# Kernel tuning notes

Measured on AMD Instinct MI355X. Metric: run time of the kernel, lower is better.

Reference implementation:

```python
import jax, jax.numpy as jnp
import numpy as np

DN = ('NCHW', 'OIHW', 'NCHW')
WINDOW_SIZES = (11, 25, 49)


def conv(x, w, b=None, pad=0, groups=1):
    y = jax.lax.conv_general_dilated(
        x, w, window_strides=(1, 1), padding=((pad, pad), (pad, pad)),
        dimension_numbers=DN, feature_group_count=groups)
    if b is not None:
        y = y + b[None, :, None, None]
    return y


def box_mean(f, wsize):
    # depthwise box-filter local mean with reflect padding (matches F.pad mode='reflect')
    C = f.shape[1]
    p = wsize // 2
    fp = jnp.pad(f, ((0, 0), (0, 0), (p, p), (p, p)), mode='reflect')
    k = jnp.ones((C, 1, wsize, wsize), f.dtype) / (wsize * wsize)
    return conv(fp, k, groups=C)


def std_map(features, wsize):
    # per-channel local std, channel-weighted sum, then **0.8
    C = features.shape[1]
    # C == 8 here, so weights are softmax(ones) == uniform (torch path for C != 4)
    cw = jax.nn.softmax(jnp.ones((C,), features.dtype))
    m = box_mean(features, wsize)
    m2 = box_mean(features ** 2, wsize)
    var = jnp.clip(m2 - m ** 2, 1e-6, None)
    res = jnp.sum(cw[None, :, None, None] * jnp.sqrt(var), axis=1, keepdims=True)
    return res ** 0.8  # [B,1,H,W]


def setup_inputs() -> dict:
    key = jax.random.key(0)
    ks = jax.random.split(key, 8)
    B, C, H, W = 8, 4, 512, 512
    x = jax.random.normal(ks[0], (B, C, H, W), dtype=jnp.float32)
    conv1_w = jax.random.normal(ks[1], (32, 4, 3, 3), dtype=jnp.float32) * 0.1
    conv1_b = jnp.zeros((32,), jnp.float32)
    conv2_w = jax.random.normal(ks[2], (16, 32, 3, 3), dtype=jnp.float32) * 0.05
    conv2_b = jnp.zeros((16,), jnp.float32)
    conv3_w = jax.random.normal(ks[3], (8, 16, 3, 3), dtype=jnp.float32) * 0.05
    conv3_b = jnp.zeros((8,), jnp.float32)
    # scale_fusion init: weight = 1/len(window_sizes), bias = 0
    fusion_w = jnp.full((1, len(WINDOW_SIZES), 1, 1), 1.0 / len(WINDOW_SIZES), jnp.float32)
    fusion_b = jnp.zeros((1,), jnp.float32)
    channel_weights = jnp.ones((4,), jnp.float32) / 4.0
    return dict(x=x, conv1_w=conv1_w, conv1_b=conv1_b, conv2_w=conv2_w,
                conv2_b=conv2_b, conv3_w=conv3_w, conv3_b=conv3_b,
                fusion_w=fusion_w, fusion_b=fusion_b,
                channel_weights=channel_weights)


def reference(x, conv1_w, conv1_b, conv2_w, conv2_b, conv3_w, conv3_b,
              fusion_w, fusion_b, channel_weights):
    lrelu = lambda v: jnp.where(v >= 0, v, 0.2 * v)
    # feature extractor: conv3x3 -> lrelu -> conv3x3 -> lrelu -> conv3x3
    f = lrelu(conv(x, conv1_w, conv1_b, pad=1))
    f = lrelu(conv(f, conv2_w, conv2_b, pad=1))
    f = conv(f, conv3_w, conv3_b, pad=1)  # [B,8,H,W]
    # multi-scale std maps
    maps = [std_map(f, w) for w in WINDOW_SIZES]
    multi = jnp.concatenate(maps, axis=1)  # [B,3,H,W]
    fused = jax.nn.relu(conv(multi, fusion_w, fusion_b, pad=0))  # [B,1,H,W]
    # adaptive thresholds (global quantiles over the whole fused std map)
    qs = jnp.quantile(fused.reshape(-1), jnp.array([0.25, 0.75], fused.dtype))
    q25, q75 = qs[0], qs[1]
    iqr = q75 - q25
    gstd = jnp.std(x, axis=(2, 3), keepdims=True, ddof=1)  # [B,4,1,1] (torch unbiased)
    lo = (q25 - 0.5 * iqr) * jnp.ones_like(gstd)
    hi = (q75 + 0.5 * iqr) * jnp.ones_like(gstd)
    gf = jnp.clip(gstd * 5.0, 0.5, 2.0)
    lo, hi = lo * gf, hi * gf
    cw = jax.nn.softmax(channel_weights)[None, :, None, None]
    cstd = jnp.std(x * cw, axis=(2, 3), keepdims=True, ddof=1)
    cf = jnp.clip(cstd * 2.0, 0.8, 1.2)
    lo, hi = lo * cf, hi * cf
    # mask generation: broadcast [B,1,H,W] vs [B,4,1,1] -> [B,4,H,W], then mean over C
    n = jnp.clip((fused - lo) / (hi - lo), 0.0, 1.0)
    mask = jax.nn.sigmoid(6.0 * n - 3.0)
    return jnp.mean(mask, axis=1, keepdims=True)  # [B,1,H,W]
```

## Files before the change

kernel.cpp:

```cpp
#include <hip/hip_runtime.h>
#include <cmath>

#define HH 512
#define WW 512
#define NB 8
#define CIN 4
#define C2 32
#define C3 16
#define CF 8
#define HW (HH*WW)
#define NPIX (NB*HW)
#define NBC 2

__device__ __forceinline__ float lrelu_f(float v){ return v < 0.f ? 0.2f*v : v; }
__device__ __forceinline__ int reflect_i(int i){ int r = i < 0 ? -i : i; return r >= HH ? 2*HH - 2 - r : r; }

template<int Ci, int Co, bool LRELU>
__global__ __launch_bounds__(256) void k_conv8(const float* __restrict__ in,
                                               const float* __restrict__ wgt,
                                               const float* __restrict__ bias,
                                               float* __restrict__ outp)
{
    constexpr int NG = Co/8;
    __shared__ float wl[Co*Ci*9];
    __shared__ float bl[Co];
    for (int i = threadIdx.x; i < Co*Ci*9; i += 256) wl[i] = wgt[i];
    if (threadIdx.x < Co) bl[threadIdx.x] = bias[threadIdx.x];
    __syncthreads();

    int bid   = blockIdx.x;
    int local = bid % (NG*128);
    int b     = bid / (NG*128);
    int cb    = local & 3;
    int rb    = (local >> 2) & 31;
    int cg    = local >> 7;
    int tid   = threadIdx.x;
    int lane  = tid & 31;
    int col   = cb*128 + lane*4;
    int row0  = rb*16  + (tid >> 5)*2;
    int co0   = cg*8;
    const float* inb = in + (size_t)b*Ci*HW;

    float acc[8][2][4];
    #pragma unroll
    for (int j=0;j<8;j++){
        float bv = bl[co0+j];
        #pragma unroll
        for (int r=0;r<2;r++)
            #pragma unroll
            for (int p=0;p<4;p++) acc[j][r][p] = bv;
    }

    #pragma unroll 2
    for (int ci=0; ci<Ci; ci++){
        float v[4][6];
        const float* inc = inb + (size_t)ci*HW;
        #pragma unroll
        for (int dy=0;dy<4;dy++){
            int hh = row0 + dy - 1;
            int hc = hh < 0 ? 0 : (hh > HH-1 ? HH-1 : hh);
            bool hok = (unsigned)hh < (unsigned)HH;
            const float* rowp = inc + hc*WW;
            float4 m = *(const float4*)(rowp + col);
            float lft = 0.f, rgt = 0.f;
            if (lane == 0  && col > 0)      lft = rowp[col-1];
            if (lane == 31 && col+4 < WW)   rgt = rowp[col+4];
            float v0 = __shfl_up(m.w, 1, 32);
            float v5 = __shfl_down(m.x, 1, 32);
            if (lane == 0)  v0 = lft;
            if (lane == 31) v5 = rgt;
            if (!hok){ m.x=0.f; m.y=0.f; m.z=0.f; m.w=0.f; v0=0.f; v5=0.f; }
            v[dy][0]=v0; v[dy][1]=m.x; v[dy][2]=m.y;
            v[dy][3]=m.z; v[dy][4]=m.w; v[dy][5]=v5;
        }
        #pragma unroll
        for (int j=0;j<8;j++){
            const float* wr = &wl[((co0+j)*Ci + ci)*9];
            float wj[9];
            #pragma unroll
            for (int q=0;q<9;q++) wj[q] = wr[q];
            #pragma unroll
            for (int dy=0;dy<3;dy++){
                #pragma unroll
                for (int dx=0;dx<3;dx++){
                    float wv = wj[dy*3+dx];
                    #pragma unroll
                    for (int r=0;r<2;r++)
                        #pragma unroll
                        for (int p=0;p<4;p++)
                            acc[j][r][p] = fmaf(v[dy+r][dx+p], wv, acc[j][r][p]);
                }
            }
        }
    }

    float* ob = outp + (size_t)b*Co*HW;
    #pragma unroll
    for (int j=0;j<8;j++){
        #pragma unroll
        for (int r=0;r<2;r++){
            float4 o;
            o.x = LRELU ? lrelu_f(acc[j][r][0]) : acc[j][r][0];
            o.y = LRELU ? lrelu_f(acc[j][r][1]) : acc[j][r][1];
            o.z = LRELU ? lrelu_f(acc[j][r][2]) : acc[j][r][2];
            o.w = LRELU ? lrelu_f(acc[j][r][3]) : acc[j][r][3];
            *(float4*)(ob + (size_t)(co0+j)*HW + (size_t)(row0+r)*WW + col) = o;
        }
    }
}

template<int WS, bool FIRST>
__global__ __launch_bounds__(256) void k_vhbox(const float* __restrict__ f,
                                               float* __restrict__ fused,
                                               const float* __restrict__ fwv, int sidx)
{
    constexpr int P    = WS/2;
    constexpr int SW   = ((256 + 2*P + 31)/32)*32;
    constexpr int SEGC = SW/32;
    constexpr int SVW  = (SW + (SW>>4) + 3) | 1;
    constexpr int RSW  = 256 + 16 + 2;
    constexpr float inv = 1.f/((float)WS*(float)WS);

    __shared__ float sv[CF*SVW];
    __shared__ float sq[CF*SVW];
    __shared__ float resv[CF*RSW];

    int bid  = blockIdx.x;
    int band = bid & 31;
    int half = (bid >> 5) & 1;
    int b    = bid >> 6;
    int r0   = band*16;
    int c0   = half*256;
    int tid  = threadIdx.x;
    int ch   = tid >> 5;
    int seg  = tid & 31;

    const float* fp = f + (size_t)(b*CF + ch)*HW;

    int rc[SEGC];
    #pragma unroll
    for (int k = 0; k < SEGC; k++){
        int gc = c0 - P + k*32 + seg;
        gc = gc < 0 ? -gc : (gc > WW-1 ? 2*WW-2 - gc : gc);
        rc[k] = gc;
    }

    float vsr[SEGC], vqr[SEGC];
    #pragma unroll
    for (int k = 0; k < SEGC; k++){ vsr[k]=0.f; vqr[k]=0.f; }
    for (int dy = -P; dy <= P; dy++){
        const float* rp = fp + (size_t)reflect_i(r0+dy)*WW;
        #pragma unroll
        for (int k = 0; k < SEGC; k++){
            float v = rp[rc[k]];
            vsr[k] += v; vqr[k] = fmaf(v, v, vqr[k]);
        }
    }

    float fwb = fwv[sidx];

    for (int rr = 0; rr < 16; rr++){
        __syncthreads();
        #pragma unroll
        for (int k = 0; k < SEGC; k++){
            int j = k*32 + seg; int sj = j + (j>>4);
            sv[ch*SVW + sj] = vsr[k];
            sq[ch*SVW + sj] = vqr[k];
        }
        float ev[SEGC], lv[SEGC];
        if (rr < 15){
            const float* ep = fp + (size_t)reflect_i(r0+rr+1+P)*WW;
            const float* lp = fp + (size_t)reflect_i(r0+rr-P)*WW;
            #pragma unroll
            for (int k = 0; k < SEGC; k++){ ev[k]=ep[rc[k]]; lv[k]=lp[rc[k]]; }
        }
        __syncthreads();
        int oc0 = seg*8;
        float S = 0.f, Q = 0.f;
        #pragma unroll
        for (int k = 0; k < WS; k++){
            int j = oc0 + k; int sj = j + (j>>4);
            S += sv[ch*SVW + sj];
            Q += sq[ch*SVW + sj];
        }
        float res[8];
        #pragma unroll
        for (int t = 0; t < 8; t++){
            float m  = S*inv, m2 = Q*inv;
            float var = fmaxf(fmaf(-m, m, m2), 1e-6f);
            res[t] = sqrtf(var);
            if (t < 7){
                int ja = oc0 + t + WS, jb = oc0 + t;
                S += sv[ch*SVW + ja + (ja>>4)] - sv[ch*SVW + jb + (jb>>4)];
                Q += sq[ch*SVW + ja + (ja>>4)] - sq[ch*SVW + jb + (jb>>4)];
            }
        }
        #pragma unroll
        for (int t = 0; t < 8; t++){
            int j = oc0 + t;
            resv[ch*RSW + j + (j>>4)] = res[t];
        }
        if (rr < 15){
            #pragma unroll
            for (int k = 0; k < SEGC; k++){
                vsr[k] += ev[k] - lv[k];
                vqr[k] = fmaf(ev[k], ev[k], vqr[k]);
                vqr[k] = fmaf(-lv[k], lv[k], vqr[k]);
            }
        }
        __syncthreads();
        int colI = tid;
        float a = 0.f;
        #pragma unroll
        for (int cc = 0; cc < CF; cc++) a += resv[cc*RSW + colI + (colI>>4)];
        float val = fwb * powf(a*0.125f, 0.8f);
        size_t oi = ((size_t)b*HH + r0 + rr)*WW + c0 + colI;
        if (FIRST) fused[oi] = val; else fused[oi] += val;
    }
}

__global__ void k_h8(const float* __restrict__ fused, const float* __restrict__ fb,
                     unsigned* __restrict__ hist8)
{
    __shared__ unsigned lh[256];
    lh[threadIdx.x] = 0;
    __syncthreads();
    float fbv = fb[0];
    int i = blockIdx.x*256 + threadIdx.x;
    int stride = gridDim.x*256;
    for (; i < NPIX; i += stride){
        float v = fmaxf(fused[i] + fbv, 0.f);
        atomicAdd(&lh[__float_as_uint(v) >> 24], 1u);
    }
    __syncthreads();
    if (lh[threadIdx.x]) atomicAdd(&hist8[threadIdx.x], lh[threadIdx.x]);
}

__global__ void k_scan8(const unsigned* __restrict__ hist8,
                        int* __restrict__ cand8, int* __restrict__ rank8)
{
    if (threadIdx.x == 0){
        const unsigned RK[4] = {524287u, 524288u, 1572863u, 1572864u};
        unsigned cum = 0; int qi = 0;
        for (int b = 0; b < 256 && qi < 4; b++){
            unsigned cnt = hist8[b];
            while (qi < 4 && RK[qi] < cum + cnt){
                cand8[qi] = b; rank8[qi] = (int)(RK[qi] - cum); qi++;
            }
            cum += cnt;
        }
    }
}

__global__ void k_h8b(const float* __restrict__ fused, const float* __restrict__ fb,
                      const int* __restrict__ cand8, unsigned* __restrict__ hist8b)
{
    __shared__ unsigned lh[1024];
    for (int i = threadIdx.x; i < 1024; i += 256) lh[i] = 0;
    __syncthreads();
    float fbv = fb[0];
    int c0 = cand8[0], c1 = cand8[1], c2 = cand8[2], c3 = cand8[3];
    bool d1 = (c1 != c0);
    bool d2 = (c2 != c0) && (c2 != c1);
    bool d3 = (c3 != c0) && (c3 != c1) && (c3 != c2);
    int i = blockIdx.x*256 + threadIdx.x;
    int stride = gridDim.x*256;
    for (; i < NPIX; i += stride){
        unsigned u = __float_as_uint(fmaxf(fused[i] + fbv, 0.f));
        int hi = (int)(u >> 24);
        unsigned mid = (u >> 16) & 0xffu;
        if (hi == c0)       atomicAdd(&lh[mid],       1u);
        if (d1 && hi == c1) atomicAdd(&lh[256u+mid],  1u);
        if (d2 && hi == c2) atomicAdd(&lh[512u+mid],  1u);
        if (d3 && hi == c3) atomicAdd(&lh[768u+mid],  1u);
    }
    __syncthreads();
    for (int i = threadIdx.x; i < 1024; i += 256)
        if (lh[i]) atomicAdd(&hist8b[i], lh[i]);
}

__global__ void k_scan8b(const unsigned* __restrict__ hist8b,
                         const int* __restrict__ cand8, const int* __restrict__ rank8,
                         int* __restrict__ cand16, int* __restrict__ rank16)
{
    int qi = threadIdx.x;
    if (qi < 4){
        int slot = qi;
        for (int j = 0; j < qi; j++) if (cand8[j] == cand8[qi]){ slot = j; break; }
        const unsigned* h = hist8b + slot*256;
        unsigned k = (unsigned)rank8[qi], cum = 0;
        for (int b = 0; b < 256; b++){
            unsigned cnt = h[b];
            if (cnt && k >= cum && k < cum + cnt){
                cand16[qi] = (cand8[qi] << 8) | b;
                rank16[qi] = (int)(k - cum);
            }
            cum += cnt;
        }
    }
}

__global__ void k_h16(const float* __restrict__ fused, const float* __restrict__ fb,
                      const int* __restrict__ cand16, unsigned* __restrict__ histlo)
{
    float fbv = fb[0];
    int c0 = cand16[0], c1 = cand16[1], c2 = cand16[2], c3 = cand16[3];
    bool d1 = (c1 != c0);
    bool d2 = (c2 != c0) && (c2 != c1);
    bool d3 = (c3 != c0) && (c3 != c1) && (c3 != c2);
    int i = blockIdx.x*256 + threadIdx.x;
    int stride = gridDim.x*256;
    for (; i < NPIX; i += stride){
        unsigned u = __float_as_uint(fmaxf(fused[i] + fbv, 0.f));
        int hi = (int)(u >> 16);
        unsigned lo = u & 0xffffu;
        if (hi == c0)       atomicAdd(&histlo[lo],           1u);
        if (d1 && hi == c1) atomicAdd(&histlo[65536u + lo],  1u);
        if (d2 && hi == c2) atomicAdd(&histlo[131072u + lo], 1u);
        if (d3 && hi == c3) atomicAdd(&histlo[196608u + lo], 1u);
    }
}

__global__ void k_scan16(const unsigned* __restrict__ histlo,
                         const int* __restrict__ cand16, const int* __restrict__ rank16,
                         float* __restrict__ ostat)
{
    int qi = blockIdx.x;
    int slot = qi;
    for (int j = 0; j < qi; j++) if (cand16[j] == cand16[qi]){ slot = j; break; }
    const unsigned* hist = histlo + (size_t)slot*65536;
    __shared__ unsigned csum[256];
    __shared__ unsigned cbase[256];
    int t = threadIdx.x;
    unsigned s = 0;
    for (int i = 0; i < 256; i++) s += hist[t*256 + i];
    csum[t] = s;
    __syncthreads();
    if (t == 0){ unsigned run = 0; for (int i = 0; i < 256; i++){ cbase[i] = run; run += csum[i]; } }
    __syncthreads();
    unsigned k = (unsigned)rank16[qi];
    unsigned cum = cbase[t];
    for (int i = 0; i < 256; i++){
        unsigned cnt = hist[t*256 + i];
        if (cnt && k >= cum && k < cum + cnt)
            ostat[qi] = __uint_as_float(((unsigned)cand16[qi] << 16) | (unsigned)(t*256 + i));
        cum += cnt;
    }
}

__global__ void k_gstd_part(const float* __restrict__ x, double* __restrict__ part)
{
    int bid = blockIdx.x;
    int plane = bid >> 3, chunk = bid & 7;
    const float4* p4 = (const float4*)(x + (size_t)plane*HW + (size_t)chunk*32768);
    int t = threadIdx.x;
    double s=0.0, s2=0.0;
    for (int k=0;k<32;k++){
        float4 v = p4[k*256 + t];
        s  += (double)v.x + (double)v.y + (double)v.z + (double)v.w;
        s2 += (double)v.x*v.x + (double)v.y*v.y + (double)v.z*v.z + (double)v.w*v.w;
    }
    __shared__ double rs[256], rq[256];
    rs[t]=s; rq[t]=s2; __syncthreads();
    for (int off=128; off>0; off>>=1){
        if (t<off){ rs[t]+=rs[t+off]; rq[t]+=rq[t+off]; }
        __syncthreads();
    }
    if (t==0){ part[bid*2]=rs[0]; part[bid*2+1]=rq[0]; }
}

__global__ void k_gstd_final(const double* __restrict__ part, float* __restrict__ gstd)
{
    int t = threadIdx.x;
    if (t < 32){
        double s=0.0, s2=0.0;
        for (int j=0;j<8;j++){ s += part[(t*8+j)*2]; s2 += part[(t*8+j)*2+1]; }
        const double N = 262144.0;
        double var = (s2 - s*s/N) / (N - 1.0);
        gstd[t] = (float)sqrt(var < 0.0 ? 0.0 : var);
    }
}

__global__ void k_finalize(const float* __restrict__ ostat, const float* __restrict__ gstd,
                           const float* __restrict__ cwin, float* __restrict__ lov, float* __restrict__ hiv)
{
    int t = threadIdx.x;
    if (t < 32){
        float q25 = ostat[0] + 0.75f*(ostat[1]-ostat[0]);
        float q75 = ostat[2] + 0.25f*(ostat[3]-ostat[2]);
        float iqr = q75 - q25;
        float lo_b = q25 - 0.5f*iqr, hi_b = q75 + 0.5f*iqr;
        int c = t & 3;
        float m = fmaxf(fmaxf(cwin[0],cwin[1]), fmaxf(cwin[2],cwin[3]));
        float e0 = expf(cwin[0]-m), e1 = expf(cwin[1]-m), e2 = expf(cwin[2]-m), e3 = expf(cwin[3]-m);
        float smc = expf(cwin[c]-m) / (e0+e1+e2+e3);
        float g  = gstd[t];
        float gf = fminf(fmaxf(g*5.f, 0.5f), 2.f);
        float cf = fminf(fmaxf(smc*g*2.f, 0.8f), 1.2f);
        lov[t] = lo_b*gf*cf;
        hiv[t] = hi_b*gf*cf;
    }
}

__global__ void k_mask(const float* __restrict__ fused_in, const float* __restrict__ fb,
                       const float* __restrict__ lov, const float* __restrict__ hiv,
                       float* __restrict__ outp)
{
    int i = blockIdx.x*256 + threadIdx.x;
    float F = fmaxf(fused_in[i] + fb[0], 0.f);
    int b = i >> 18;
    float o = 0.f;
    #pragma unroll
    for (int c=0;c<4;c++){
        float lo = lov[b*4+c], hi = hiv[b*4+c];
        float n = (F - lo) / (hi - lo);
        n = fminf(fmaxf(n, 0.f), 1.f);
        o += 1.f/(1.f + expf(3.f - 6.f*n));
    }
    outp[i] = 0.25f * o;
}

extern "C" void kernel_launch(void* const* d_in, const int* in_sizes, int n_in,
                              void* d_out, int out_size, void* d_ws, size_t ws_size,
                              hipStream_t stream)
{
    const float* x  = (const float*)d_in[0];
    const float* w1 = (const float*)d_in[1];
    const float* b1 = (const float*)d_in[2];
    const float* w2 = (const float*)d_in[3];
    const float* b2 = (const float*)d_in[4];
    const float* w3 = (const float*)d_in[5];
    const float* b3 = (const float*)d_in[6];
    const float* fw = (const float*)d_in[7];
    const float* fb = (const float*)d_in[8];
    const float* cw = (const float*)d_in[9];
    float* out = (float*)d_out;
    char* ws = (char*)d_ws;

    size_t off = 0;
    auto take = [&](size_t bytes)->size_t{ size_t o = off; off += (bytes + 255) & ~(size_t)255; return o; };
    size_t o_h8     = take(256*4);
    size_t o_h8b    = take(1024*4);
    size_t o_histlo = take((size_t)4*65536*4);
    size_t o_c8     = take(4*4);
    size_t o_r8     = take(4*4);
    size_t o_c16    = take(4*4);
    size_t o_r16    = take(4*4);
    size_t o_os     = take(4*4);
    size_t o_part   = take(512*8);
    size_t o_gs     = take(32*4);
    size_t o_lo     = take(32*4);
    size_t o_hi     = take(32*4);
    size_t o_R1     = take((size_t)NB*C3*HW*4);
    size_t o_R2     = take((size_t)NBC*C2*HW*4);

    float*    f2buf  = (float*)(ws + o_R1);
    float*    f1     = (float*)(ws + o_R2);
    float*    fbuf   = (float*)(ws + o_R2);
    unsigned* hist8  = (unsigned*)(ws + o_h8);
    unsigned* hist8b = (unsigned*)(ws + o_h8b);
    unsigned* histlo = (unsigned*)(ws + o_histlo);
    int*      c8     = (int*)(ws + o_c8);
    int*      r8     = (int*)(ws + o_r8);
    int*      c16    = (int*)(ws + o_c16);
    int*      r16    = (int*)(ws + o_r16);
    float*    osv    = (float*)(ws + o_os);
    double*   part   = (double*)(ws + o_part);
    float*    gs     = (float*)(ws + o_gs);
    float*    lov    = (float*)(ws + o_lo);
    float*    hiv    = (float*)(ws + o_hi);

    for (int ck = 0; ck < NB/NBC; ck++){
        const float* xb = x + (size_t)ck*NBC*CIN*HW;
        k_conv8<CIN,C2,true ><<<NBC*512,256,0,stream>>>(xb, w1, b1, f1);
        k_conv8<C2, C3,true ><<<NBC*256,256,0,stream>>>(f1, w2, b2,
                                                        f2buf + (size_t)ck*NBC*C3*HW);
    }
    k_conv8<C3, CF, false><<<NB*128,256,0,stream>>>(f2buf, w3, b3, fbuf);

    k_gstd_part<<<256,256,0,stream>>>(x, part);
    k_gstd_final<<<1,256,0,stream>>>(part, gs);

    const int bgrid = NB*2*32;
    k_vhbox<11,true ><<<bgrid,256,0,stream>>>(fbuf, out, fw, 0);
    k_vhbox<25,false><<<bgrid,256,0,stream>>>(fbuf, out, fw, 1);
    k_vhbox<49,false><<<bgrid,256,0,stream>>>(fbuf, out, fw, 2);

    hipMemsetAsync(hist8,  0, 256*4,  stream);
    hipMemsetAsync(hist8b, 0, 1024*4, stream);
    hipMemsetAsync(histlo, 0, (size_t)4*65536*4, stream);
    k_h8    <<<2048,256,0,stream>>>(out, fb, hist8);
    k_scan8 <<<1,64,0,stream>>>(hist8, c8, r8);
    k_h8b   <<<2048,256,0,stream>>>(out, fb, c8, hist8b);
    k_scan8b<<<1,64,0,stream>>>(hist8b, c8, r8, c16, r16);
    k_h16   <<<2048,256,0,stream>>>(out, fb, c16, histlo);
    k_scan16<<<4,256,0,stream>>>(histlo, c16, r16, osv);

    k_finalize<<<1,64,0,stream>>>(osv, gs, cw, lov, hiv);
    k_mask<<<NPIX/256,256,0,stream>>>(out, fb, lov, hiv, out);
}
```

Before: 905.9 us.

## Fuse three std-map scales into one kernel and shrink conv tiles

The three per-scale box-filter std kernels are merged into one kernel that reads a shared 320-wide padded strip and keeps running column sums for all three windows. This removes two passes over the feature map and the read-modify-write of the fused output. The conv kernels now compute one row per thread instead of two, doubling the grid, and conv3 runs inside the batch-chunk loop so intermediates stay smaller. The three histogram memsets are also collapsed into one. The cost is higher register pressure in the fused std kernel, plus lost row reuse in the conv kernels.

```diff
diff --git a/kernel.cpp b/kernel.cpp
--- a/kernel.cpp
+++ b/kernel.cpp
@@ -12,11 +12,17 @@
 #define NPIX (NB*HW)
 #define NBC 2
 
+#define SEGC 10
+#define SW   320
+#define SVW  ((SW + (SW>>4) + 3) | 1)
+#define RSW  (256 + 16 + 2)
+
 __device__ __forceinline__ float lrelu_f(float v){ return v < 0.f ? 0.2f*v : v; }
 __device__ __forceinline__ int reflect_i(int i){ int r = i < 0 ? -i : i; return r >= HH ? 2*HH - 2 - r : r; }
+__device__ __forceinline__ int swz(int j){ return j + (j >> 4); }
 
 template<int Ci, int Co, bool LRELU>
-__global__ __launch_bounds__(256) void k_conv8(const float* __restrict__ in,
+__global__ __launch_bounds__(256) void k_conv4(const float* __restrict__ in,
                                                const float* __restrict__ wgt,
                                                const float* __restrict__ bias,
                                                float* __restrict__ outp)
@@ -29,42 +35,40 @@
     __syncthreads();
 
     int bid   = blockIdx.x;
-    int local = bid % (NG*128);
-    int b     = bid / (NG*128);
+    int local = bid % (NG*256);
+    int b     = bid / (NG*256);
     int cb    = local & 3;
-    int rb    = (local >> 2) & 31;
-    int cg    = local >> 7;
+    int rb    = (local >> 2) & 63;
+    int cg    = local >> 8;
     int tid   = threadIdx.x;
     int lane  = tid & 31;
     int col   = cb*128 + lane*4;
-    int row0  = rb*16  + (tid >> 5)*2;
+    int row   = rb*8 + (tid >> 5);
     int co0   = cg*8;
     const float* inb = in + (size_t)b*Ci*HW;
 
-    float acc[8][2][4];
+    float acc[8][4];
     #pragma unroll
     for (int j=0;j<8;j++){
         float bv = bl[co0+j];
         #pragma unroll
-        for (int r=0;r<2;r++)
-            #pragma unroll
-            for (int p=0;p<4;p++) acc[j][r][p] = bv;
+        for (int p=0;p<4;p++) acc[j][p] = bv;
     }
 
     #pragma unroll 2
     for (int ci=0; ci<Ci; ci++){
-        float v[4][6];
+        float v[3][6];
         const float* inc = inb + (size_t)ci*HW;
         #pragma unroll
-        for (int dy=0;dy<4;dy++){
-            int hh = row0 + dy - 1;
+        for (int dy=0;dy<3;dy++){
+            int hh = row + dy - 1;
             int hc = hh < 0 ? 0 : (hh > HH-1 ? HH-1 : hh);
             bool hok = (unsigned)hh < (unsigned)HH;
             const float* rowp = inc + hc*WW;
             float4 m = *(const float4*)(rowp + col);
             float lft = 0.f, rgt = 0.f;
-            if (lane == 0  && col > 0)      lft = rowp[col-1];
-            if (lane == 31 && col+4 < WW)   rgt = rowp[col+4];
+            if (lane == 0  && col > 0)    lft = rowp[col-1];
+            if (lane == 31 && col+4 < WW) rgt = rowp[col+4];
             float v0 = __shfl_up(m.w, 1, 32);
             float v5 = __shfl_down(m.x, 1, 32);
             if (lane == 0)  v0 = lft;
@@ -85,10 +89,8 @@
                 for (int dx=0;dx<3;dx++){
                     float wv = wj[dy*3+dx];
                     #pragma unroll
-                    for (int r=0;r<2;r++)
-                        #pragma unroll
-                        for (int p=0;p<4;p++)
-                            acc[j][r][p] = fmaf(v[dy+r][dx+p], wv, acc[j][r][p]);
+                    for (int p=0;p<4;p++)
+                        acc[j][p] = fmaf(v[dy][dx+p], wv, acc[j][p]);
                 }
             }
         }
@@ -97,33 +99,71 @@
     float* ob = outp + (size_t)b*Co*HW;
     #pragma unroll
     for (int j=0;j<8;j++){
-        #pragma unroll
-        for (int r=0;r<2;r++){
-            float4 o;
-            o.x = LRELU ? lrelu_f(acc[j][r][0]) : acc[j][r][0];
-            o.y = LRELU ? lrelu_f(acc[j][r][1]) : acc[j][r][1];
-            o.z = LRELU ? lrelu_f(acc[j][r][2]) : acc[j][r][2];
-            o.w = LRELU ? lrelu_f(acc[j][r][3]) : acc[j][r][3];
-            *(float4*)(ob + (size_t)(co0+j)*HW + (size_t)(row0+r)*WW + col) = o;
-        }
-    }
-}
-
-template<int WS, bool FIRST>
-__global__ __launch_bounds__(256) void k_vhbox(const float* __restrict__ f,
-                                               float* __restrict__ fused,
-                                               const float* __restrict__ fwv, int sidx)
-{
-    constexpr int P    = WS/2;
-    constexpr int SW   = ((256 + 2*P + 31)/32)*32;
-    constexpr int SEGC = SW/32;
-    constexpr int SVW  = (SW + (SW>>4) + 3) | 1;
-    constexpr int RSW  = 256 + 16 + 2;
+        float4 o;
+        o.x = LRELU ? lrelu_f(acc[j][0]) : acc[j][0];
+        o.y = LRELU ? lrelu_f(acc[j][1]) : acc[j][1];
+        o.z = LRELU ? lrelu_f(acc[j][2]) : acc[j][2];
+        o.w = LRELU ? lrelu_f(acc[j][3]) : acc[j][3];
+        *(float4*)(ob + (size_t)(co0+j)*HW + (size_t)row*WW + col) = o;
+    }
+}
+
+template<int WS>
+__device__ __forceinline__ float scale_step(float2* __restrict__ svq,
+                                            float* __restrict__ resv,
+                                            const float* vs, const float* vq,
+                                            float fws)
+{
+    constexpr int P   = WS/2;
+    constexpr int OFF = 24 - P;
     constexpr float inv = 1.f/((float)WS*(float)WS);
-
-    __shared__ float sv[CF*SVW];
-    __shared__ float sq[CF*SVW];
-    __shared__ float resv[CF*RSW];
+    const int tid = threadIdx.x;
+    const int ch  = tid >> 5;
+    const int seg = tid & 31;
+
+    __syncthreads();
+    #pragma unroll
+    for (int k=0;k<SEGC;k++){
+        int j = k*32 + seg;
+        svq[ch*SVW + swz(j)] = make_float2(vs[k], vq[k]);
+    }
+    __syncthreads();
+
+    int base = OFF + seg*8;
+    float S = 0.f, Q = 0.f;
+    #pragma unroll
+    for (int q=0;q<WS;q++){
+        float2 t = svq[ch*SVW + swz(base+q)];
+        S += t.x; Q += t.y;
+    }
+    float res[8];
+    #pragma unroll
+    for (int t8=0;t8<8;t8++){
+        float m = S*inv, m2 = Q*inv;
+        res[t8] = sqrtf(fmaxf(fmaf(-m, m, m2), 1e-6f));
+        if (t8 < 7){
+            float2 ta = svq[ch*SVW + swz(base+t8+WS)];
+            float2 tb = svq[ch*SVW + swz(base+t8)];
+            S += ta.x - tb.x; Q += ta.y - tb.y;
+        }
+    }
+    #pragma unroll
+    for (int t8=0;t8<8;t8++)
+        resv[ch*RSW + swz(seg*8+t8)] = res[t8];
+    __syncthreads();
+
+    float a = 0.f;
+    #pragma unroll
+    for (int cc=0;cc<CF;cc++) a += resv[cc*RSW + swz(tid)];
+    return fws * powf(a*0.125f, 0.8f);
+}
+
+__global__ __launch_bounds__(256) void k_std3(const float* __restrict__ f,
+                                              float* __restrict__ fused,
+                                              const float* __restrict__ fwv)
+{
+    __shared__ float2 svq[CF*SVW];
+    __shared__ float  resv[CF*RSW];
 
     int bid  = blockIdx.x;
     int band = bid & 31;
@@ -134,88 +174,73 @@
     int tid  = threadIdx.x;
     int ch   = tid >> 5;
     int seg  = tid & 31;
-
     const float* fp = f + (size_t)(b*CF + ch)*HW;
 
     int rc[SEGC];
     #pragma unroll
-    for (int k = 0; k < SEGC; k++){
-        int gc = c0 - P + k*32 + seg;
+    for (int k=0;k<SEGC;k++){
+        int gc = c0 - 24 + k*32 + seg;
         gc = gc < 0 ? -gc : (gc > WW-1 ? 2*WW-2 - gc : gc);
         rc[k] = gc;
     }
 
-    float vsr[SEGC], vqr[SEGC];
-    #pragma unroll
-    for (int k = 0; k < SEGC; k++){ vsr[k]=0.f; vqr[k]=0.f; }
-    for (int dy = -P; dy <= P; dy++){
+    float vs49[SEGC], vq49[SEGC], vs25[SEGC], vq25[SEGC], vs11[SEGC], vq11[SEGC];
+    #pragma unroll
+    for (int k=0;k<SEGC;k++){
+        vs49[k]=0.f; vq49[k]=0.f; vs25[k]=0.f; vq25[k]=0.f; vs11[k]=0.f; vq11[k]=0.f;
+    }
+    #pragma unroll 1
+    for (int dy=-24; dy<=24; dy++){
         const float* rp = fp + (size_t)reflect_i(r0+dy)*WW;
+        bool in25 = (dy >= -12 && dy <= 12);
+        bool in11 = (dy >= -5  && dy <= 5);
         #pragma unroll
-        for (int k = 0; k < SEGC; k++){
-            float v = rp[rc[k]];
-            vsr[k] += v; vqr[k] = fmaf(v, v, vqr[k]);
-        }
-    }
-
-    float fwb = fwv[sidx];
-
-    for (int rr = 0; rr < 16; rr++){
-        __syncthreads();
-        #pragma unroll
-        for (int k = 0; k < SEGC; k++){
-            int j = k*32 + seg; int sj = j + (j>>4);
-            sv[ch*SVW + sj] = vsr[k];
-            sq[ch*SVW + sj] = vqr[k];
-        }
-        float ev[SEGC], lv[SEGC];
+        for (int k=0;k<SEGC;k++){
+            float v = rp[rc[k]]; float v2 = v*v;
+            vs49[k] += v; vq49[k] += v2;
+            if (in25){ vs25[k] += v; vq25[k] += v2; }
+            if (in11){ vs11[k] += v; vq11[k] += v2; }
+        }
+    }
+
+    float fw0 = fwv[0], fw1 = fwv[1], fw2 = fwv[2];
+
+    for (int rr=0; rr<16; rr++){
+        int r = r0 + rr;
+        float val;
+        val  = scale_step<11>(svq, resv, vs11, vq11, fw0);
+        val += scale_step<25>(svq, resv, vs25, vq25, fw1);
+        val += scale_step<49>(svq, resv, vs49, vq49, fw2);
+        fused[((size_t)b*HH + r)*WW + c0 + tid] = val;
         if (rr < 15){
-            const float* ep = fp + (size_t)reflect_i(r0+rr+1+P)*WW;
-            const float* lp = fp + (size_t)reflect_i(r0+rr-P)*WW;
-            #pragma unroll
-            for (int k = 0; k < SEGC; k++){ ev[k]=ep[rc[k]]; lv[k]=lp[rc[k]]; }
-        }
-        __syncthreads();
-        int oc0 = seg*8;
-        float S = 0.f, Q = 0.f;
-        #pragma unroll
-        for (int k = 0; k < WS; k++){
-            int j = oc0 + k; int sj = j + (j>>4);
-            S += sv[ch*SVW + sj];
-            Q += sq[ch*SVW + sj];
-        }
-        float res[8];
-        #pragma unroll
-        for (int t = 0; t < 8; t++){
-            float m  = S*inv, m2 = Q*inv;
-            float var = fmaxf(fmaf(-m, m, m2), 1e-6f);
-            res[t] = sqrtf(var);
-            if (t < 7){
-                int ja = oc0 + t + WS, jb = oc0 + t;
-                S += sv[ch*SVW + ja + (ja>>4)] - sv[ch*SVW + jb + (jb>>4)];
-                Q += sq[ch*SVW + ja + (ja>>4)] - sq[ch*SVW + jb + (jb>>4)];
+            {   const float* ep = fp + (size_t)reflect_i(r+1+24)*WW;
+                const float* lp = fp + (size_t)reflect_i(r-24)*WW;
+                #pragma unroll
+                for (int k=0;k<SEGC;k++){
+                    float e = ep[rc[k]], l = lp[rc[k]];
+                    vs49[k] += e - l;
+                    vq49[k] = fmaf(e, e, vq49[k]); vq49[k] = fmaf(-l, l, vq49[k]);
+                }
             }
-        }
-        #pragma unroll
-        for (int t = 0; t < 8; t++){
-            int j = oc0 + t;
-            resv[ch*RSW + j + (j>>4)] = res[t];
-        }
-        if (rr < 15){
-            #pragma unroll
-            for (int k = 0; k < SEGC; k++){
-                vsr[k] += ev[k] - lv[k];
-                vqr[k] = fmaf(ev[k], ev[k], vqr[k]);
-                vqr[k] = fmaf(-lv[k], lv[k], vqr[k]);
+            {   const float* ep = fp + (size_t)reflect_i(r+1+12)*WW;
+                const float* lp = fp + (size_t)reflect_i(r-12)*WW;
+                #pragma unroll
+                for (int k=0;k<SEGC;k++){
+                    float e = ep[rc[k]], l = lp[rc[k]];
+                    vs25[k] += e - l;
+                    vq25[k] = fmaf(e, e, vq25[k]); vq25[k] = fmaf(-l, l, vq25[k]);
+                }
             }
-        }
-        __syncthreads();
-        int colI = tid;
-        float a = 0.f;
-        #pragma unroll
-        for (int cc = 0; cc < CF; cc++) a += resv[cc*RSW + colI + (colI>>4)];
-        float val = fwb * powf(a*0.125f, 0.8f);
-        size_t oi = ((size_t)b*HH + r0 + rr)*WW + c0 + colI;
-        if (FIRST) fused[oi] = val; else fused[oi] += val;
+            {   const float* ep = fp + (size_t)reflect_i(r+1+5)*WW;
+                const float* lp = fp + (size_t)reflect_i(r-5)*WW;
+                #pragma unroll
+                for (int k=0;k<SEGC;k++){
+                    float e = ep[rc[k]], l = lp[rc[k]];
+                    vs11[k] += e - l;
+                    vq11[k] = fmaf(e, e, vq11[k]); vq11[k] = fmaf(-l, l, vq11[k]);
+                }
+            }
+        }
     }
 }
 
@@ -451,12 +476,13 @@
     size_t o_gs     = take(32*4);
     size_t o_lo     = take(32*4);
     size_t o_hi     = take(32*4);
-    size_t o_R1     = take((size_t)NB*C3*HW*4);
-    size_t o_R2     = take((size_t)NBC*C2*HW*4);
-
-    float*    f2buf  = (float*)(ws + o_R1);
-    float*    f1     = (float*)(ws + o_R2);
-    float*    fbuf   = (float*)(ws + o_R2);
+    size_t o_f1     = take((size_t)NBC*C2*HW*4);
+    size_t o_f2c    = take((size_t)NBC*C3*HW*4);
+    size_t o_fb     = take((size_t)NB*CF*HW*4);
+
+    float*    f1     = (float*)(ws + o_f1);
+    float*    f2c    = (float*)(ws + o_f2c);
+    float*    fbuf   = (float*)(ws + o_fb);
     unsigned* hist8  = (unsigned*)(ws + o_h8);
     unsigned* hist8b = (unsigned*)(ws + o_h8b);
     unsigned* histlo = (unsigned*)(ws + o_histlo);
@@ -469,26 +495,22 @@
     float*    gs     = (float*)(ws + o_gs);
     float*    lov    = (float*)(ws + o_lo);
     float*    hiv    = (float*)(ws + o_hi);
+    size_t hist_bytes = (o_histlo + (size_t)4*65536*4) - o_h8;
 
     for (int ck = 0; ck < NB/NBC; ck++){
-        const float* xb = x + (size_t)ck*NBC*CIN*HW;
-        k_conv8<CIN,C2,true ><<<NBC*512,256,0,stream>>>(xb, w1, b1, f1);
-        k_conv8<C2, C3,true ><<<NBC*256,256,0,stream>>>(f1, w2, b2,
-                                                        f2buf + (size_t)ck*NBC*C3*HW);
-    }
-    k_conv8<C3, CF, false><<<NB*128,256,0,stream>>>(f2buf, w3, b3, fbuf);
+        const float* xb = x    + (size_t)ck*NBC*CIN*HW;
+        float*       fo = fbuf + (size_t)ck*NBC*CF*HW;
+        k_conv4<CIN,C2,true ><<<NBC*1024,256,0,stream>>>(xb,  w1, b1, f1);
+        k_conv4<C2, C3,true ><<<NBC*512, 256,0,stream>>>(f1,  w2, b2, f2c);
+        k_conv4<C3, CF,false><<<NBC*256, 256,0,stream>>>(f2c, w3, b3, fo);
+    }
 
     k_gstd_part<<<256,256,0,stream>>>(x, part);
     k_gstd_final<<<1,256,0,stream>>>(part, gs);
 
-    const int bgrid = NB*2*32;
-    k_vhbox<11,true ><<<bgrid,256,0,stream>>>(fbuf, out, fw, 0);
-    k_vhbox<25,false><<<bgrid,256,0,stream>>>(fbuf, out, fw, 1);
-    k_vhbox<49,false><<<bgrid,256,0,stream>>>(fbuf, out, fw, 2);
-
-    hipMemsetAsync(hist8,  0, 256*4,  stream);
-    hipMemsetAsync(hist8b, 0, 1024*4, stream);
-    hipMemsetAsync(histlo, 0, (size_t)4*65536*4, stream);
+    k_std3<<<NB*2*32,256,0,stream>>>(fbuf, out, fw);
+
+    hipMemsetAsync(hist8, 0, hist_bytes, stream);
     k_h8    <<<2048,256,0,stream>>>(out, fb, hist8);
     k_scan8 <<<1,64,0,stream>>>(hist8, c8, r8);
     k_h8b   <<<2048,256,0,stream>>>(out, fb, c8, hist8b);
```

Measured after the change: 1.028 ms. 13.5% more time.
